# Optimization experiments

Hardware: AMD Instinct MI355X
Metric: run time of the kernel (lower is better)

Reference implementation:

```python
import jax, jax.numpy as jnp
import numpy as np
import math

B, S, D, H = 2, 2048, 1024, 16
DK = D // H

def setup_inputs() -> dict:
    key = jax.random.key(0)
    ks = jax.random.split(key, 12)
    def xavier(k, shape):
        fan_in, fan_out = shape[1], shape[0]
        limit = math.sqrt(6.0 / (fan_in + fan_out))
        return jax.random.uniform(k, shape, jnp.float32, -limit, limit)
    inp = {
        'query': jax.random.normal(ks[0], (B, S, D), jnp.float32),
        'key':   jax.random.normal(ks[1], (B, S, D), jnp.float32),
        'value': jax.random.normal(ks[2], (B, S, D), jnp.float32),
        # causal mask, broadcast over heads: (B, 1, S, S), 1 = keep, 0 = mask
        'mask':  jnp.broadcast_to(jnp.tril(jnp.ones((S, S), jnp.int32)), (B, 1, S, S)),
        'Wq': xavier(ks[3], (D, D)), 'bq': jnp.zeros((D,), jnp.float32),
        'Wk': xavier(ks[4], (D, D)), 'bk': jnp.zeros((D,), jnp.float32),
        'Wv': xavier(ks[5], (D, D)), 'bv': jnp.zeros((D,), jnp.float32),
        'Wo': xavier(ks[6], (D, D)), 'bo': jnp.zeros((D,), jnp.float32),
    }
    return inp

def _split_heads(x):
    # (B, S, D) -> (B, H, S, DK)
    b, s, _ = x.shape
    return x.reshape(b, s, H, DK).transpose(0, 2, 1, 3)

def reference(query, key, value, mask, Wq, bq, Wk, bk, Wv, bv, Wo, bo):
    # torch nn.Linear: y = x @ W.T + b
    Q = _split_heads(query @ Wq.T + bq)   # (B,H,S,DK)
    K = _split_heads(key   @ Wk.T + bk)
    V = _split_heads(value @ Wv.T + bv)
    scores = jnp.einsum('bhqd,bhkd->bhqk', Q, K) / math.sqrt(DK)  # (B,H,S,S)
    scores = jnp.where(mask == 0, jnp.float32(-1e9), scores)
    attn = jax.nn.softmax(scores, axis=-1)  # dropout p=0 -> identity
    out = jnp.einsum('bhqk,bhkd->bhqd', attn, V)  # (B,H,S,DK)
    out = out.transpose(0, 2, 1, 3).reshape(query.shape[0], query.shape[1], D)
    return out @ Wo.T + bo
```

## Files before the change

kernel.cpp:

```cpp
#include <hip/hip_runtime.h>
#include <hip/hip_bf16.h>
#include <type_traits>


typedef __attribute__((ext_vector_type(8))) short short8;
typedef __attribute__((ext_vector_type(4))) short s16x4;
typedef __attribute__((ext_vector_type(4))) float floatx4;

__device__ __forceinline__ short f2bf(float x) {
    union { float f; unsigned u; } v; v.f = x;
    unsigned r = v.u + 0x7fffu + ((v.u >> 16) & 1u);
    return (short)(r >> 16);
}

__device__ __forceinline__ unsigned pk2bf(float a, float b) {
    union { __hip_bfloat162 h2; unsigned u; } cv;
    cv.h2 = __float22bfloat162_rn(make_float2(a, b));
    return cv.u;
}

__device__ __forceinline__ float fast_exp2(float x) {
#if __has_builtin(__builtin_amdgcn_exp2f)
    return __builtin_amdgcn_exp2f(x);
#else
    return __expf(x * 0.69314718056f);
#endif
}

typedef __attribute__((address_space(3))) short lds_short;
typedef __attribute__((address_space(1))) const short glb_short;
__device__ __forceinline__ void load_lds16(const void* g, void* l) {
    __builtin_amdgcn_global_load_lds((glb_short*)g, (lds_short*)l, 16, 0, 0);
}

__global__ __launch_bounds__(256) void cvt_all(
        const float* __restrict__ q, const float* __restrict__ k,
        const float* __restrict__ v,
        const float* __restrict__ wq, const float* __restrict__ wk,
        const float* __restrict__ wv, const float* __restrict__ wo,
        unsigned short* __restrict__ xq, unsigned short* __restrict__ xk,
        unsigned short* __restrict__ xv,
        unsigned short* __restrict__ wqb, unsigned short* __restrict__ wkb,
        unsigned short* __restrict__ wvb, unsigned short* __restrict__ wob) {
    const float* s; unsigned short* d;
    int bx = blockIdx.x;
    switch (blockIdx.y) {
        case 0: s = q; d = xq; break;
        case 1: s = k; d = xk; break;
        case 2: s = v; d = xv; break;
        default: {
            int wsel = bx >> 9; bx &= 511;
            s = (wsel == 0) ? wq : (wsel == 1) ? wk : (wsel == 2) ? wv : wo;
            d = (wsel == 0) ? wqb : (wsel == 1) ? wkb : (wsel == 2) ? wvb : wob;
        }
    }
    size_t i = ((size_t)bx * 256 + threadIdx.x) * 8;
    floatx4 a = *(const floatx4*)(s + i), b2 = *(const floatx4*)(s + i + 4);
    union { unsigned u[4]; short8 v8; } o;
    o.u[0] = pk2bf(a[0], a[1]);  o.u[1] = pk2bf(a[2], a[3]);
    o.u[2] = pk2bf(b2[0], b2[1]); o.u[3] = pk2bf(b2[2], b2[3]);
    *(short8*)(d + i) = o.v8;
}

__global__ __launch_bounds__(256, 6) void gemm_qkv(
        const unsigned short* __restrict__ Xq, const unsigned short* __restrict__ Xk,
        const unsigned short* __restrict__ Xv,
        const unsigned short* __restrict__ Wq, const unsigned short* __restrict__ Wk,
        const unsigned short* __restrict__ Wv,
        const float* __restrict__ bq, const float* __restrict__ bk,
        const float* __restrict__ bv,
        unsigned short* __restrict__ Qb, unsigned short* __restrict__ Kb,
        unsigned short* __restrict__ Vb) {
    constexpr int K = 1024, N = 1024;
    __shared__ short As[64 * 64];
    __shared__ short Bs[128 * 64];
    const int t = threadIdx.x;
    const int slot = blockIdx.x;
    const int p = (slot & 7) + 8 * (slot >> 6);
    const int nx = (slot >> 3) & 7;
    const int chunk = p >> 6, my = p & 63;
    const unsigned short* A = chunk == 0 ? Xq : chunk == 1 ? Xk : Xv;
    const unsigned short* W = chunk == 0 ? Wq : chunk == 1 ? Wk : Wv;
    const float* bias        = chunk == 0 ? bq : chunk == 1 ? bk : bv;
    unsigned short* Y        = chunk == 0 ? Qb : chunk == 1 ? Kb : Vb;
    const float scale = chunk == 0 ? 0.1803368801f : 1.0f;
    const int m0 = my * 64, n0 = nx * 128;
    const int lane = t & 63, w = t >> 6;
    const int l16 = lane & 15, quad = lane >> 4;
    const int srow8 = t >> 3, scs8 = t & 7;
    floatx4 acc[4][2] = {};

    for (int k0 = 0; k0 < K; k0 += 64) {
        __syncthreads();
        for (int i = 0; i < 2; i++) {
            const int row = i * 32 + srow8;
            const int cg = scs8 ^ (row & 7);
            load_lds16(A + (size_t)(m0 + row) * K + k0 + cg * 8, &As[i * 2048 + t * 8]);
        }
        for (int i = 0; i < 4; i++) {
            const int row = i * 32 + srow8;
            const int cg = scs8 ^ (row & 7);
            load_lds16(W + (size_t)(n0 + row) * K + k0 + cg * 8, &Bs[i * 2048 + t * 8]);
        }
        __syncthreads();

        for (int kc = 0; kc < 2; kc++) {
            short8 af[4], bf[2];
            for (int ms = 0; ms < 4; ms++) {
                const int row = ms * 16 + l16;
                af[ms] = *(short8*)&As[row * 64 + (((kc << 2) | quad) ^ (row & 7)) * 8];
            }
            for (int ns = 0; ns < 2; ns++) {
                const int row = w * 32 + ns * 16 + l16;
                bf[ns] = *(short8*)&Bs[row * 64 + (((kc << 2) | quad) ^ (row & 7)) * 8];
            }
            for (int ms = 0; ms < 4; ms++)
                for (int ns = 0; ns < 2; ns++)
                    acc[ms][ns] = __builtin_amdgcn_mfma_f32_16x16x32_bf16(
                            af[ms], bf[ns], acc[ms][ns], 0, 0, 0);
        }
    }

    for (int ms = 0; ms < 4; ms++)
        for (int ns = 0; ns < 2; ns++) {
            int col = n0 + w * 32 + ns * 16 + l16;
            float bb = bias[col];
            for (int r = 0; r < 4; r++) {
                int row = m0 + ms * 16 + quad * 4 + r;
                Y[(size_t)row * N + col] =
                    (unsigned short)f2bf((acc[ms][ns][r] + bb) * scale);
            }
        }
}

__global__ __launch_bounds__(256, 4) void gemm_o(
        const unsigned short* __restrict__ A, const unsigned short* __restrict__ W,
        const float* __restrict__ bo, float* __restrict__ out) {
    constexpr int K = 1024, N = 1024;
    __shared__ short As[64 * 64];
    __shared__ short Bs[64 * 64];
    const int t = threadIdx.x;
    const int slot = blockIdx.x;
    const int p = (slot & 7) + 8 * (slot >> 7);
    const int nx = (slot >> 3) & 15;
    const int m0 = p * 64, n0 = nx * 64;
    const int lane = t & 63, w = t >> 6;
    const int l16 = lane & 15, quad = lane >> 4;
    const int wm = w >> 1, wn = w & 1;
    const int srow8 = t >> 3, scs8 = t & 7;
    floatx4 acc[2][2] = {};

    for (int k0 = 0; k0 < K; k0 += 64) {
        __syncthreads();
        for (int i = 0; i < 2; i++) {
            const int row = i * 32 + srow8;
            const int cg = scs8 ^ (row & 7);
            load_lds16(A + (size_t)(m0 + row) * K + k0 + cg * 8, &As[i * 2048 + t * 8]);
            load_lds16(W + (size_t)(n0 + row) * K + k0 + cg * 8, &Bs[i * 2048 + t * 8]);
        }
        __syncthreads();

        for (int kc = 0; kc < 2; kc++) {
            short8 af[2], bf[2];
            for (int ms = 0; ms < 2; ms++) {
                const int row = wm * 32 + ms * 16 + l16;
                af[ms] = *(short8*)&As[row * 64 + (((kc << 2) | quad) ^ (row & 7)) * 8];
            }
            for (int ns = 0; ns < 2; ns++) {
                const int row = wn * 32 + ns * 16 + l16;
                bf[ns] = *(short8*)&Bs[row * 64 + (((kc << 2) | quad) ^ (row & 7)) * 8];
            }
            for (int ms = 0; ms < 2; ms++)
                for (int ns = 0; ns < 2; ns++)
                    acc[ms][ns] = __builtin_amdgcn_mfma_f32_16x16x32_bf16(
                            af[ms], bf[ns], acc[ms][ns], 0, 0, 0);
        }
    }

    for (int ms = 0; ms < 2; ms++)
        for (int ns = 0; ns < 2; ns++) {
            int col = n0 + wn * 32 + ns * 16 + l16;
            float bb = bo[col];
            for (int r = 0; r < 4; r++) {
                int row = m0 + wm * 32 + ms * 16 + quad * 4 + r;
                out[(size_t)row * N + col] = acc[ms][ns][r] + bb;
            }
        }
}

__global__ __launch_bounds__(256) void attn_kernel(
        const unsigned short* __restrict__ Q, const unsigned short* __restrict__ Kp,
        const unsigned short* __restrict__ Vp, unsigned short* __restrict__ O) {
    __shared__ short Ks[64 * 72];
    __shared__ short Vt[64 * 72];
    __shared__ short Ps[4][16 * 72];
    const int t = threadIdx.x;
    const int bx = blockIdx.x;
    const int g = bx >> 8, c = bx & 255;
    const int dlt = c >> 5, bh = c & 31;
    const int unit = (g == 0) ? 31 - dlt : (g == 1) ? 23 - dlt
                   : (g == 2) ? 8 + dlt  : dlt;
    const int h = bh & 15, b = bh >> 4;
    const int q0 = unit * 64;
    const int lane = t & 63, w = t >> 6, l16 = lane & 15, quad = lane >> 4;
    const int krow = t >> 2, kcg = (t & 3) * 16;
    const int vp2 = t & 31, vg = t >> 5;

    short8 qf[2];
    {
        const size_t base = ((size_t)(b * 2048 + q0 + w * 16 + l16)) * 1024 + h * 64;
        qf[0] = *(const short8*)(Q + base + quad * 8);
        qf[1] = *(const short8*)(Q + base + 32 + quad * 8);
    }
    float l = 0.f;
    floatx4 o[4] = {};

    short8 ka, kb, va, vc;
    {
        const size_t kbse = ((size_t)(b * 2048 + krow)) * 1024 + h * 64 + kcg;
        ka = *(const short8*)(Kp + kbse);
        kb = *(const short8*)(Kp + kbse + 8);
        const size_t vbse = ((size_t)(b * 2048 + 2 * vp2)) * 1024 + h * 64 + vg * 8;
        va = *(const short8*)(Vp + vbse);
        vc = *(const short8*)(Vp + vbse + 1024);
    }

    for (int kv0 = 0; kv0 <= q0; kv0 += 64) {
        __syncthreads();
        *(short8*)&Ks[krow * 72 + kcg] = ka;
        *(short8*)&Ks[krow * 72 + kcg + 8] = kb;
        for (int i = 0; i < 8; i++) {
            unsigned pk = (unsigned)(unsigned short)va[i] |
                          ((unsigned)(unsigned short)vc[i] << 16);
            *(unsigned*)&Vt[(vg * 8 + i) * 72 + 2 * vp2] = pk;
        }
        __syncthreads();

        if (kv0 < q0) {
            const size_t kbse = ((size_t)(b * 2048 + kv0 + 64 + krow)) * 1024 + h * 64 + kcg;
            ka = *(const short8*)(Kp + kbse);
            kb = *(const short8*)(Kp + kbse + 8);
            const size_t vbse = ((size_t)(b * 2048 + kv0 + 64 + 2 * vp2)) * 1024 + h * 64 + vg * 8;
            va = *(const short8*)(Vp + vbse);
            vc = *(const short8*)(Vp + vbse + 1024);
        }

        floatx4 sv[4] = {};
        __builtin_amdgcn_s_setprio(1);
        for (int hh = 0; hh < 4; hh++)
            for (int kc = 0; kc < 2; kc++) {
                short8 kf = *(short8*)&Ks[(hh * 16 + l16) * 72 + kc * 32 + quad * 8];
                sv[hh] = __builtin_amdgcn_mfma_f32_16x16x32_bf16(kf, qf[kc], sv[hh], 0, 0, 0);
            }
        __builtin_amdgcn_s_setprio(0);

        {
            const bool needmask = (kv0 + 63 > q0 + w * 16);
            const int qg = q0 + w * 16 + l16;
            float ls = 0.f;
            for (int hh = 0; hh < 4; hh++) {
                float pv[4];
                for (int r = 0; r < 4; r++) {
                    int kv = kv0 + hh * 16 + quad * 4 + r;
                    float e = fast_exp2(sv[hh][r]);
                    pv[r] = (needmask && kv > qg) ? 0.f : e;
                    ls += pv[r];
                }
                union { unsigned u[2]; s16x4 v4; } pw;
                pw.u[0] = pk2bf(pv[0], pv[1]); pw.u[1] = pk2bf(pv[2], pv[3]);
                *(s16x4*)&Ps[w][l16 * 72 + hh * 16 + quad * 4] = pw.v4;
            }
            ls += __shfl_xor(ls, 16);
            ls += __shfl_xor(ls, 32);
            l += ls;
        }

        short8 p0 = *(short8*)&Ps[w][l16 * 72 + quad * 8];
        short8 p1 = *(short8*)&Ps[w][l16 * 72 + 32 + quad * 8];
        __builtin_amdgcn_s_setprio(1);
        for (int nc = 0; nc < 4; nc++) {
            short8 vf0 = *(short8*)&Vt[(nc * 16 + l16) * 72 + quad * 8];
            short8 vf1 = *(short8*)&Vt[(nc * 16 + l16) * 72 + 32 + quad * 8];
            o[nc] = __builtin_amdgcn_mfma_f32_16x16x32_bf16(vf0, p0, o[nc], 0, 0, 0);
            o[nc] = __builtin_amdgcn_mfma_f32_16x16x32_bf16(vf1, p1, o[nc], 0, 0, 0);
        }
        __builtin_amdgcn_s_setprio(0);
    }

    const float rl = 1.f / l;
    const size_t orow = ((size_t)(b * 2048 + q0 + w * 16 + l16)) * 1024 + h * 64;
    for (int nc = 0; nc < 4; nc++) {
        union { unsigned u[2]; s16x4 v4; } ow;
        ow.u[0] = pk2bf(o[nc][0] * rl, o[nc][1] * rl);
        ow.u[1] = pk2bf(o[nc][2] * rl, o[nc][3] * rl);
        *(s16x4*)(O + orow + nc * 16 + quad * 4) = ow.v4;
    }
}

extern "C" void kernel_launch(void* const* d_in, const int* in_sizes, int n_in,
                              void* d_out, int out_size, void* d_ws, size_t ws_size,
                              hipStream_t stream) {
    const float* query = (const float*)d_in[0];
    const float* key   = (const float*)d_in[1];
    const float* value = (const float*)d_in[2];
    const float* Wq = (const float*)d_in[4];
    const float* bq = (const float*)d_in[5];
    const float* Wk = (const float*)d_in[6];
    const float* bk = (const float*)d_in[7];
    const float* Wv = (const float*)d_in[8];
    const float* bv = (const float*)d_in[9];
    const float* Wo = (const float*)d_in[10];
    const float* bo = (const float*)d_in[11];

    const size_t NE = (size_t)4096 * 1024;
    const size_t WE = (size_t)1024 * 1024;
    unsigned short* Xq  = (unsigned short*)d_ws;
    unsigned short* Xk  = Xq + NE;
    unsigned short* Xv  = Xk + NE;
    unsigned short* Qb  = Xv + NE;
    unsigned short* Kb  = Qb + NE;
    unsigned short* Vb  = Kb + NE;
    unsigned short* Ob  = Vb + NE;
    unsigned short* Wqb = Ob + NE;
    unsigned short* Wkb = Wqb + WE;
    unsigned short* Wvb = Wkb + WE;
    unsigned short* Wob = Wvb + WE;

    cvt_all<<<dim3(2048, 4), 256, 0, stream>>>(query, key, value, Wq, Wk, Wv, Wo,
                                               Xq, Xk, Xv, Wqb, Wkb, Wvb, Wob);
    gemm_qkv<<<dim3(1536), 256, 0, stream>>>(Xq, Xk, Xv, Wqb, Wkb, Wvb,
                                             bq, bk, bv, Qb, Kb, Vb);
    attn_kernel<<<dim3(1024), 256, 0, stream>>>(Qb, Kb, Vb, Ob);
    gemm_o<<<dim3(1024), 256, 0, stream>>>(Ob, Wob, bo, (float*)d_out);
}
```

Baseline: 231.0 us.

## Write V projection pre-transposed per head so attention loads V^T directly

The QKV projection GEMM now writes the V output (chunk 2) in a per-(batch,head) transposed layout [b][h][dk][seq], using packed 4-element bf16 stores. The attention kernel then loads V^T rows contiguously and stores them straight into shared memory with vector writes. This replaces the per-element pack-and-scatter transpose into LDS on every KV tile. The cost is moved to the GEMM epilogue, whose stores to the transposed layout are strided across columns.

```diff
diff --git a/kernel.cpp b/kernel.cpp
--- a/kernel.cpp
+++ b/kernel.cpp
@@ -121,16 +121,31 @@
         }
     }
 
-    for (int ms = 0; ms < 4; ms++)
-        for (int ns = 0; ns < 2; ns++) {
-            int col = n0 + w * 32 + ns * 16 + l16;
-            float bb = bias[col];
-            for (int r = 0; r < 4; r++) {
-                int row = m0 + ms * 16 + quad * 4 + r;
-                Y[(size_t)row * N + col] =
-                    (unsigned short)f2bf((acc[ms][ns][r] + bb) * scale);
-            }
-        }
+    if (chunk == 2) {
+        for (int ms = 0; ms < 4; ms++)
+            for (int ns = 0; ns < 2; ns++) {
+                const int col = n0 + w * 32 + ns * 16 + l16;
+                const float bb = bias[col];
+                const int row0 = m0 + ms * 16 + quad * 4;
+                const size_t dst = ((size_t)((row0 >> 11) * 16 + (col >> 6)) * 64
+                                    + (col & 63)) * 2048 + (row0 & 2047);
+                union { unsigned u[2]; s16x4 v4; } ow;
+                ow.u[0] = pk2bf(acc[ms][ns][0] + bb, acc[ms][ns][1] + bb);
+                ow.u[1] = pk2bf(acc[ms][ns][2] + bb, acc[ms][ns][3] + bb);
+                *(s16x4*)(Y + dst) = ow.v4;
+            }
+    } else {
+        for (int ms = 0; ms < 4; ms++)
+            for (int ns = 0; ns < 2; ns++) {
+                int col = n0 + w * 32 + ns * 16 + l16;
+                float bb = bias[col];
+                for (int r = 0; r < 4; r++) {
+                    int row = m0 + ms * 16 + quad * 4 + r;
+                    Y[(size_t)row * N + col] =
+                        (unsigned short)f2bf((acc[ms][ns][r] + bb) * scale);
+                }
+            }
+    }
 }
 
 __global__ __launch_bounds__(256, 4) void gemm_o(
@@ -204,7 +219,6 @@
     const int q0 = unit * 64;
     const int lane = t & 63, w = t >> 6, l16 = lane & 15, quad = lane >> 4;
     const int krow = t >> 2, kcg = (t & 3) * 16;
-    const int vp2 = t & 31, vg = t >> 5;
 
     short8 qf[2];
     {
@@ -215,34 +229,31 @@
     float l = 0.f;
     floatx4 o[4] = {};
 
+    const size_t vtbase = ((size_t)((b * 16 + h) * 64 + krow)) * 2048;
+
     short8 ka, kb, va, vc;
     {
         const size_t kbse = ((size_t)(b * 2048 + krow)) * 1024 + h * 64 + kcg;
         ka = *(const short8*)(Kp + kbse);
         kb = *(const short8*)(Kp + kbse + 8);
-        const size_t vbse = ((size_t)(b * 2048 + 2 * vp2)) * 1024 + h * 64 + vg * 8;
-        va = *(const short8*)(Vp + vbse);
-        vc = *(const short8*)(Vp + vbse + 1024);
+        va = *(const short8*)(Vp + vtbase + kcg);
+        vc = *(const short8*)(Vp + vtbase + kcg + 8);
     }
 
     for (int kv0 = 0; kv0 <= q0; kv0 += 64) {
         __syncthreads();
         *(short8*)&Ks[krow * 72 + kcg] = ka;
         *(short8*)&Ks[krow * 72 + kcg + 8] = kb;
-        for (int i = 0; i < 8; i++) {
-            unsigned pk = (unsigned)(unsigned short)va[i] |
-                          ((unsigned)(unsigned short)vc[i] << 16);
-            *(unsigned*)&Vt[(vg * 8 + i) * 72 + 2 * vp2] = pk;
-        }
+        *(short8*)&Vt[krow * 72 + kcg] = va;
+        *(short8*)&Vt[krow * 72 + kcg + 8] = vc;
         __syncthreads();
 
         if (kv0 < q0) {
             const size_t kbse = ((size_t)(b * 2048 + kv0 + 64 + krow)) * 1024 + h * 64 + kcg;
             ka = *(const short8*)(Kp + kbse);
             kb = *(const short8*)(Kp + kbse + 8);
-            const size_t vbse = ((size_t)(b * 2048 + kv0 + 64 + 2 * vp2)) * 1024 + h * 64 + vg * 8;
-            va = *(const short8*)(Vp + vbse);
-            vc = *(const short8*)(Vp + vbse + 1024);
+            va = *(const short8*)(Vp + vtbase + kv0 + 64 + kcg);
+            vc = *(const short8*)(Vp + vtbase + kv0 + 64 + kcg + 8);
         }
 
         floatx4 sv[4] = {};
```

New measurement: 227.3 us. About the same (-1.6%).
